# Optimization experiments

Hardware: AMD Instinct MI355X
Metric: run time of the kernel (lower is better)

## Reference

```python
import jax, jax.numpy as jnp
import numpy as np

B, S, DIM = 2, 2048, 2048
H, QLR, KVLR = 16, 1536, 512
D_NOPE, D_ROPE, D_QK, D_V = 128, 64, 192, 128
EPS = 1e-6


def rms_norm(x, w, eps=EPS):
    return x * jax.lax.rsqrt(jnp.mean(jnp.square(x), axis=-1, keepdims=True) + eps) * w


def rope(x, theta):
    # x: [b, s, n, d], theta: [s, d//2] rotation angles
    xr = x.reshape(*x.shape[:-1], -1, 2)
    x0, x1 = xr[..., 0], xr[..., 1]
    cos = jnp.cos(theta)[None, :, None, :]
    sin = jnp.sin(theta)[None, :, None, :]
    out = jnp.stack([x0 * cos - x1 * sin, x0 * sin + x1 * cos], axis=-1)
    return out.reshape(x.shape).astype(x.dtype)


def setup_inputs() -> dict:
    key = jax.random.key(0)
    ks = jax.random.split(key, 6)
    x = jax.random.normal(ks[0], (B, S, DIM), jnp.float32)
    # standard RoPE angles theta[s, i] = s / 10000^(2i/d_rope)
    pos = jnp.arange(S, dtype=jnp.float32)
    inv = 1.0 / (10000.0 ** (jnp.arange(0, D_ROPE, 2, dtype=jnp.float32) / D_ROPE))
    freqs = pos[:, None] * inv[None, :]  # [S, D_ROPE//2]
    sc = lambda k, shp: jax.random.normal(k, shp, jnp.float32) * (1.0 / np.sqrt(shp[0]))
    return {
        'x': x,
        'freqs': freqs,
        'start_pos': 0,
        'wq_a': sc(ks[1], (DIM, QLR)),
        'q_norm_w': jnp.ones((QLR,), jnp.float32),
        'wq_b': sc(ks[2], (QLR, H * D_QK)),
        'wkv_a': sc(ks[3], (DIM, KVLR + D_ROPE)),
        'kv_norm_w': jnp.ones((KVLR,), jnp.float32),
        'wkv_b': sc(ks[4], (KVLR, H * (D_NOPE + D_V))),
        'wo': sc(ks[5], (H * D_V, DIM)),
    }


def reference(x, freqs, start_pos, wq_a, q_norm_w, wq_b, wkv_a, kv_norm_w, wkv_b, wo):
    bsz, seqlen, _ = x.shape
    scale = D_QK ** -0.5
    # low-rank Q: down-proj -> RMSNorm -> up-proj
    q = rms_norm(x @ wq_a, q_norm_w) @ wq_b
    q = q.reshape(bsz, seqlen, H, D_QK)
    q_nope, q_pe = q[..., :D_NOPE], q[..., D_NOPE:]
    q_pe = rope(q_pe, freqs)
    # low-rank KV: joint down-proj, split latent / rope part
    kv = x @ wkv_a
    c_kv, k_pe = kv[..., :KVLR], kv[..., KVLR:]
    k_pe = rope(k_pe[:, :, None, :], freqs)[:, :, 0, :]  # [b, t, r]
    # weight absorption: fold wkv_b's k_nope block into q
    wkv_b_mat = wkv_b.T.reshape(H, D_NOPE + D_V, KVLR)  # [h, d_nope+d_v, c]
    q_abs = jnp.einsum('bshd,hdc->bshc', q_nope, wkv_b_mat[:, :D_NOPE])
    kv_cache = rms_norm(c_kv, kv_norm_w)  # [b, t, c] compressed KV cache
    scores = (jnp.einsum('bshc,btc->bsht', q_abs, kv_cache)
              + jnp.einsum('bshr,btr->bsht', q_pe, k_pe)) * scale
    causal = jnp.tril(jnp.ones((seqlen, seqlen), bool))  # prefill, start_pos=0
    scores = jnp.where(causal[None, :, None, :], scores, -1e9)
    attn = jax.nn.softmax(scores.astype(jnp.float32), axis=-1).astype(x.dtype)
    # attend in latent space, then up-project with the v block of wkv_b
    o = jnp.einsum('bsht,btc->bshc', attn, kv_cache)
    o = jnp.einsum('bshc,hdc->bshd', o, wkv_b_mat[:, D_NOPE:])
    return o.reshape(bsz, seqlen, H * D_V) @ wo
```

## Files before the change

kernel.cpp:

```cpp
#include <hip/hip_runtime.h>

typedef __bf16 bf16x8 __attribute__((ext_vector_type(8)));
typedef float floatx4 __attribute__((ext_vector_type(4)));

#define MFMA(a, b, c) __builtin_amdgcn_mfma_f32_16x16x32_bf16((a), (b), (c), 0, 0, 0)

__device__ __forceinline__ float bf2f(ushort u) {
    union { unsigned int i; float f; } v; v.i = ((unsigned int)u) << 16; return v.f;
}
__device__ __forceinline__ ushort f2bf(float f) {
    union { float f; unsigned int i; } v; v.f = f;
    unsigned int r = v.i + 0x7fffu + ((v.i >> 16) & 1u);
    return (ushort)(r >> 16);
}
__device__ __forceinline__ ushort f2bf_n(float f) {
    union { __bf16 b; ushort u; } v; v.b = (__bf16)f; return v.u;
}
__device__ __forceinline__ bf16x8 ldb8(const ushort* p) { return *(const bf16x8*)p; }

__global__ __launch_bounds__(256) void transpose_f32_bf16(
    const float* __restrict__ in, ushort* __restrict__ out, int R, int C) {
    __shared__ ushort tile[32][33];
    const int c0 = blockIdx.x * 32, r0 = blockIdx.y * 32;
    const int tx = threadIdx.x, ty = threadIdx.y;
    #pragma unroll
    for (int i = 0; i < 32; i += 8) {
        int r = r0 + ty + i, c = c0 + tx;
        if (r < R && c < C) tile[ty + i][tx] = f2bf(in[(long)r * C + c]);
    }
    __syncthreads();
    #pragma unroll
    for (int i = 0; i < 32; i += 8) {
        int r = c0 + ty + i, c = r0 + tx;
        if (r < C && c < R) out[(long)r * R + c] = tile[tx][ty + i];
    }
}

__global__ __launch_bounds__(256) void cvt_f32_bf16(
    const float* __restrict__ in, ushort* __restrict__ out, long n) {
    const long i = ((long)blockIdx.x * 256 + threadIdx.x) * 4;
    if (i >= n) return;
    float4 v = *(const float4*)(in + i);
    ushort4 o;
    o.x = f2bf(v.x); o.y = f2bf(v.y); o.z = f2bf(v.z); o.w = f2bf(v.w);
    *(ushort4*)(out + i) = o;
}

__global__ __launch_bounds__(256) void trigtab(
    const float* __restrict__ freqs, float2* __restrict__ trig) {
    const int idx = blockIdx.x * 256 + threadIdx.x;
    float th = freqs[idx];
    trig[idx] = make_float2(cosf(th), sinf(th));
}

__global__ __launch_bounds__(256, 3) void gemm_bt128(
    const ushort* __restrict__ A, const ushort* __restrict__ Bt,
    void* __restrict__ C, int K, int lda, int ldb, int ldc,
    long aZ, long bZ, long cZ, int c_f32) {
    __shared__ __align__(16) ushort As[128 * 64];
    __shared__ __align__(16) ushort Bs[128 * 64];
    const int z = blockIdx.z;
    const ushort* Ab = A + (long)z * aZ;
    const ushort* Bb = Bt + (long)z * bZ;
    const long m0 = (long)blockIdx.y * 128;
    const long n0 = (long)blockIdx.x * 128;
    const int tid = threadIdx.x;
    const int lane = tid & 63, w = tid >> 6;
    const int wm = (w >> 1) * 64, wn = (w & 1) * 64;
    const int lrow = lane & 15, quad = lane >> 4;

    floatx4 acc[4][4] = {};

    for (int k0 = 0; k0 < K; k0 += 64) {
        __syncthreads();
        #pragma unroll
        for (int t = 0; t < 4; ++t) {
            const int c = t * 256 + tid;
            const int r = c >> 3, kc = (c & 7) * 8;
            __builtin_amdgcn_global_load_lds(
                (const __attribute__((address_space(1))) unsigned int*)(Ab + (m0 + r) * lda + k0 + kc),
                (__attribute__((address_space(3))) unsigned int*)(As + (long)c * 8), 16, 0, 0);
            __builtin_amdgcn_global_load_lds(
                (const __attribute__((address_space(1))) unsigned int*)(Bb + (n0 + r) * ldb + k0 + kc),
                (__attribute__((address_space(3))) unsigned int*)(Bs + (long)c * 8), 16, 0, 0);
        }
        __syncthreads();
        #pragma unroll
        for (int kk = 0; kk < 64; kk += 32) {
            bf16x8 af[4], bv[4];
            #pragma unroll
            for (int i = 0; i < 4; ++i) {
                af[i] = ldb8(&As[(wm + i * 16 + lrow) * 64 + kk + quad * 8]);
                bv[i] = ldb8(&Bs[(wn + i * 16 + lrow) * 64 + kk + quad * 8]);
            }
            #pragma unroll
            for (int i = 0; i < 4; ++i)
                #pragma unroll
                for (int j = 0; j < 4; ++j)
                    acc[i][j] = MFMA(af[i], bv[j], acc[i][j]);
        }
    }
    if (c_f32) {
        float* Cb = (float*)C + (long)z * cZ;
        #pragma unroll
        for (int mt = 0; mt < 4; ++mt)
            #pragma unroll
            for (int nt = 0; nt < 4; ++nt)
                #pragma unroll
                for (int r = 0; r < 4; ++r)
                    Cb[(m0 + wm + mt * 16 + quad * 4 + r) * ldc + n0 + wn + nt * 16 + lrow] = acc[mt][nt][r];
    } else {
        ushort* Cb = (ushort*)C + (long)z * cZ;
        #pragma unroll
        for (int mt = 0; mt < 4; ++mt)
            #pragma unroll
            for (int nt = 0; nt < 4; ++nt)
                #pragma unroll
                for (int r = 0; r < 4; ++r)
                    Cb[(m0 + wm + mt * 16 + quad * 4 + r) * ldc + n0 + wn + nt * 16 + lrow] = f2bf(acc[mt][nt][r]);
    }
}

__global__ __launch_bounds__(256) void rms1536(
    ushort* qk, const float* __restrict__ w) {
    const int row = blockIdx.x, t = threadIdx.x;
    const int lane = t & 63, wv = t >> 6;
    ushort* ip = qk + (long)row * 2176;
    float v[6]; float ss = 0.f;
    #pragma unroll
    for (int i = 0; i < 6; ++i) { v[i] = bf2f(ip[i * 256 + t]); ss += v[i] * v[i]; }
    #pragma unroll
    for (int off = 32; off > 0; off >>= 1) ss += __shfl_xor(ss, off);
    __shared__ float red[4];
    if (lane == 0) red[wv] = ss;
    __syncthreads();
    const float tot = red[0] + red[1] + red[2] + red[3];
    const float sc = rsqrtf(tot * (1.f / 1536.f) + 1e-6f);
    #pragma unroll
    for (int i = 0; i < 6; ++i) ip[i * 256 + t] = f2bf(v[i] * sc * w[i * 256 + t]);
}

__global__ __launch_bounds__(256) void qrope(
    const ushort* __restrict__ q, const float2* __restrict__ trig,
    ushort* __restrict__ qpe) {
    const int tok = blockIdx.x;
    const int s = tok & 2047;
    const int t = threadIdx.x;
    #pragma unroll
    for (int p = 0; p < 2; ++p) {
        const int idx = p * 256 + t;
        const int h = idx >> 5, i = idx & 31;
        const long base = (long)tok * 3072 + h * 192 + 128 + 2 * i;
        float x0 = bf2f(q[base]), x1 = bf2f(q[base + 1]);
        float2 cs = trig[s * 32 + i];
        const long ob = (long)tok * 1024 + h * 64 + 2 * i;
        qpe[ob]     = f2bf(x0 * cs.x - x1 * cs.y);
        qpe[ob + 1] = f2bf(x0 * cs.y + x1 * cs.x);
    }
}

__global__ __launch_bounds__(256) void kvprep(
    const ushort* __restrict__ qk, const float* __restrict__ w,
    const float2* __restrict__ trig, ushort* __restrict__ kvc,
    ushort* __restrict__ kpe) {
    const int tok = blockIdx.x;
    const int s = tok & 2047;
    const int t = threadIdx.x;
    const int lane = t & 63, wv = t >> 6;
    const ushort* in2 = qk + (long)tok * 2176 + 1536;
    const float v0 = bf2f(in2[t]);
    const float v1 = bf2f(in2[256 + t]);
    float ss = v0 * v0 + v1 * v1;
    #pragma unroll
    for (int off = 32; off > 0; off >>= 1) ss += __shfl_xor(ss, off);
    __shared__ float red[4];
    if (lane == 0) red[wv] = ss;
    __syncthreads();
    const float tot = red[0] + red[1] + red[2] + red[3];
    const float sc = rsqrtf(tot * (1.f / 512.f) + 1e-6f);
    kvc[(long)tok * 512 + t] = f2bf(v0 * sc * w[t]);
    kvc[(long)tok * 512 + 256 + t] = f2bf(v1 * sc * w[256 + t]);
    if (t < 32) {
        float x0 = bf2f(in2[512 + 2 * t]);
        float x1 = bf2f(in2[512 + 2 * t + 1]);
        float2 cs = trig[s * 32 + t];
        kpe[(long)tok * 64 + 2 * t]     = f2bf(x0 * cs.x - x1 * cs.y);
        kpe[(long)tok * 64 + 2 * t + 1] = f2bf(x0 * cs.y + x1 * cs.x);
    }
}

__global__ __launch_bounds__(256, 2) void mha_attn(
    const ushort* __restrict__ q,
    const ushort* __restrict__ qpe,
    const ushort* __restrict__ kn,
    const ushort* __restrict__ kpe,
    const ushort* __restrict__ vT,
    ushort* __restrict__ o2) {
    __shared__ __align__(16) ushort Ks[128][200];
    __shared__ __align__(16) ushort P[64][136];
    const int fid = blockIdx.x + (blockIdx.y << 4) + (blockIdx.z << 8);
    const int xcd = fid & 7, j = fid >> 3;
    const int g = xcd * 4 + (j >> 4);
    const int qx = j & 15, h = g & 15, b = g >> 4;
    const int tid = threadIdx.x, lane = tid & 63, w = tid >> 6;
    const int lrow = lane & 15, quad = lane >> 4;
    const long bb = (long)b * 2048;
    const float scale = 0.07216878364870323f * 1.4426950408889634f;
    const int rn = tid >> 4, cn = (tid & 15) * 8;
    const int rr = tid >> 3, cr = (tid & 7) * 8;

    for (int half = 0; half < 2; ++half) {
        const int qt = half ? (31 - qx) : qx;
        const int qrow = qt * 64;
        const long tokb = bb + qrow;

        bf16x8 qa[6];
        {
            const ushort* qp_ = q + (tokb + w * 16 + lrow) * 3072 + h * 192 + quad * 8;
            #pragma unroll
            for (int ks = 0; ks < 4; ++ks) qa[ks] = ldb8(qp_ + ks * 32);
            const ushort* qq = qpe + (tokb + w * 16 + lrow) * 1024 + h * 64 + quad * 8;
            qa[4] = ldb8(qq); qa[5] = ldb8(qq + 32);
        }

        floatx4 oacc[4][2] = {};
        float m_i[4], l_i[4];
        #pragma unroll
        for (int r = 0; r < 4; ++r) { m_i[r] = -1e30f; l_i[r] = 0.f; }

        const int niter = qt / 2 + 1;
        for (int t = 0; t < niter; ++t) {
            const int kv0 = t * 128;
            {
                const ushort* src = kn + (bb + kv0 + rn) * 2048 + h * 128 + cn;
                #pragma unroll
                for (int j2 = 0; j2 < 8; ++j2) {
                    uint4 v = *(const uint4*)(src + (long)j2 * 16 * 2048);
                    *(uint4*)&Ks[j2 * 16 + rn][cn] = v;
                }
                const ushort* srp = kpe + (bb + kv0 + rr) * 64 + cr;
                #pragma unroll
                for (int j2 = 0; j2 < 4; ++j2) {
                    uint4 v = *(const uint4*)(srp + (long)j2 * 32 * 64);
                    *(uint4*)&Ks[j2 * 32 + rr][128 + cr] = v;
                }
            }
            __syncthreads();

            floatx4 sacc[8] = {};
            __builtin_amdgcn_s_setprio(1);
            #pragma unroll
            for (int f = 0; f < 8; ++f)
                #pragma unroll
                for (int ks = 0; ks < 6; ++ks)
                    sacc[f] = MFMA(qa[ks], ldb8(&Ks[f * 16 + lrow][ks * 32 + quad * 8]), sacc[f]);
            __builtin_amdgcn_s_setprio(0);

            bf16x8 vf[2][4];
            {
                const ushort* vb = vT + ((long)(b * 16 + h)) * 262144 + (long)(w * 32 + lrow) * 2048 + kv0 + quad * 8;
                #pragma unroll
                for (int nf = 0; nf < 2; ++nf)
                    #pragma unroll
                    for (int kk = 0; kk < 4; ++kk)
                        vf[nf][kk] = ldb8(vb + (long)nf * 16 * 2048 + kk * 32);
            }

            const bool diag = (t == niter - 1);
            #pragma unroll
            for (int r = 0; r < 4; ++r) {
                const int rloc = w * 16 + quad * 4 + r;
                const int row_s = qrow + rloc;
                float pv[8];
                float smax = -1e30f;
                #pragma unroll
                for (int f = 0; f < 8; ++f) {
                    pv[f] = sacc[f][r] * scale;
                    if (diag) { if (kv0 + f * 16 + lrow > row_s) pv[f] = -1e30f; }
                    smax = fmaxf(smax, pv[f]);
                }
                #pragma unroll
                for (int off = 1; off < 16; off <<= 1)
                    smax = fmaxf(smax, __shfl_xor(smax, off));
                const float mnew = fmaxf(m_i[r], smax);
                const float alpha = __builtin_amdgcn_exp2f(m_i[r] - mnew);
                float ps = 0.f;
                #pragma unroll
                for (int f = 0; f < 8; ++f) {
                    float p = __builtin_amdgcn_exp2f(pv[f] - mnew);
                    P[rloc][f * 16 + lrow] = f2bf_n(p);
                    ps += p;
                }
                #pragma unroll
                for (int off = 1; off < 16; off <<= 1)
                    ps += __shfl_xor(ps, off);
                l_i[r] = l_i[r] * alpha + ps;
                m_i[r] = mnew;
                if (lrow == 0) *(float*)&P[rloc][128] = alpha;
            }
            __syncthreads();

            __builtin_amdgcn_s_setprio(1);
            #pragma unroll
            for (int mf = 0; mf < 4; ++mf) {
                float al[4];
                #pragma unroll
                for (int r = 0; r < 4; ++r) al[r] = *(const float*)&P[mf * 16 + quad * 4 + r][128];
                const int need = (al[0] != 1.f) | (al[1] != 1.f) | (al[2] != 1.f) | (al[3] != 1.f);
                if (__any(need)) {
                    #pragma unroll
                    for (int nf = 0; nf < 2; ++nf)
                        #pragma unroll
                        for (int r = 0; r < 4; ++r) oacc[mf][nf][r] *= al[r];
                }
                #pragma unroll
                for (int kk = 0; kk < 4; ++kk) {
                    bf16x8 pf = ldb8(&P[mf * 16 + lrow][kk * 32 + quad * 8]);
                    oacc[mf][0] = MFMA(pf, vf[0][kk], oacc[mf][0]);
                    oacc[mf][1] = MFMA(pf, vf[1][kk], oacc[mf][1]);
                }
            }
            __builtin_amdgcn_s_setprio(0);
        }

        #pragma unroll
        for (int r = 0; r < 4; ++r)
            if (lrow == 0) *(float*)&P[w * 16 + quad * 4 + r][132] = l_i[r];
        __syncthreads();
        #pragma unroll
        for (int mf = 0; mf < 4; ++mf) {
            float li[4];
            #pragma unroll
            for (int r = 0; r < 4; ++r) li[r] = *(const float*)&P[mf * 16 + quad * 4 + r][132];
            #pragma unroll
            for (int nf = 0; nf < 2; ++nf)
                #pragma unroll
                for (int r = 0; r < 4; ++r) {
                    long tok = tokb + mf * 16 + quad * 4 + r;
                    o2[tok * 2048 + h * 128 + w * 32 + nf * 16 + lrow] = f2bf_n(oacc[mf][nf][r] / li[r]);
                }
        }
        __syncthreads();
    }
}

extern "C" void kernel_launch(void* const* d_in, const int* in_sizes, int n_in,
                              void* d_out, int out_size, void* d_ws, size_t ws_size,
                              hipStream_t stream) {
    const float* x      = (const float*)d_in[0];
    const float* freqs  = (const float*)d_in[1];
    const float* wq_a   = (const float*)d_in[3];
    const float* qnw    = (const float*)d_in[4];
    const float* wq_b   = (const float*)d_in[5];
    const float* wkv_a  = (const float*)d_in[6];
    const float* kvnw   = (const float*)d_in[7];
    const float* wkv_b  = (const float*)d_in[8];
    const float* wo     = (const float*)d_in[9];
    float* out = (float*)d_out;
    (void)ws_size; (void)in_sizes; (void)n_in; (void)out_size;

    char* ws = (char*)d_ws;
    ushort* qk_comb = (ushort*)(ws + 0);
    ushort* o2      = (ushort*)(ws + 0);
    ushort* xb      = (ushort*)(ws + 17825792);
    ushort* knope   = (ushort*)(ws + 17825792);
    ushort* q       = (ushort*)(ws + 34603008);
    ushort* qpe     = (ushort*)(ws + 59768832);
    ushort* kvc     = (ushort*)(ws + 68157440);
    ushort* kpe     = (ushort*)(ws + 72351744);
    ushort* vT      = (ushort*)(ws + 72876032);
    ushort* wcombT  = (ushort*)(ws + 89653248);
    ushort* wq_bT   = (ushort*)(ws + 98566144);
    ushort* wkv_bT  = (ushort*)(ws + 108003328);
    ushort* woT     = (ushort*)(ws + 112197632);
    float2* trig    = (float2*)(ws + 120586240);

    dim3 tb(32, 8);
    trigtab<<<256, 256, 0, stream>>>(freqs, trig);
    transpose_f32_bf16<<<dim3(48, 64), tb, 0, stream>>>(wq_a, wcombT, 2048, 1536);
    transpose_f32_bf16<<<dim3(18, 64), tb, 0, stream>>>(wkv_a, wcombT + 1536L * 2048, 2048, 576);
    transpose_f32_bf16<<<dim3(96, 48), tb, 0, stream>>>(wq_b, wq_bT, 1536, 3072);
    transpose_f32_bf16<<<dim3(128, 16), tb, 0, stream>>>(wkv_b, wkv_bT, 512, 4096);
    transpose_f32_bf16<<<dim3(64, 64), tb, 0, stream>>>(wo, woT, 2048, 2048);
    cvt_f32_bf16<<<8192, 256, 0, stream>>>(x, xb, 8388608L);

    gemm_bt128<<<dim3(17, 32, 1), 256, 0, stream>>>(xb, wcombT, qk_comb, 2048, 2048, 2048, 2176, 0, 0, 0, 0);
    rms1536<<<4096, 256, 0, stream>>>(qk_comb, qnw);
    gemm_bt128<<<dim3(24, 32, 1), 256, 0, stream>>>(qk_comb, wq_bT, q, 1536, 2176, 1536, 3072, 0, 0, 0, 0);
    qrope<<<4096, 256, 0, stream>>>(q, trig, qpe);
    kvprep<<<4096, 256, 0, stream>>>(qk_comb, kvnw, trig, kvc, kpe);

    gemm_bt128<<<dim3(1, 32, 16), 256, 0, stream>>>(kvc, wkv_bT, knope,
        512, 512, 512, 2048, 0, 131072, 128, 0);
    gemm_bt128<<<dim3(16, 1, 16), 256, 0, stream>>>(wkv_bT + 65536, kvc, vT,
        512, 512, 512, 2048, 131072, 0, 262144, 0);
    gemm_bt128<<<dim3(16, 1, 16), 256, 0, stream>>>(wkv_bT + 65536, kvc + 1048576, vT + 4194304,
        512, 512, 512, 2048, 131072, 0, 262144, 0);

    mha_attn<<<dim3(16, 16, 2), 256, 0, stream>>>(q, qpe, knope, kpe, vT, o2);

    gemm_bt128<<<dim3(16, 32, 1), 256, 0, stream>>>(o2, woT, out, 2048, 2048, 2048, 2048, 0, 0, 0, 1);
}
```

Measured before the change: 479.3 us.

## Merge per-batch V up-projection GEMMs and add lazy softmax max rescaling

Replaces the two per-batch V-projection GEMM launches with one dedicated gemm_vt kernel that covers both batches through blockIdx.z, loading tiles into LDS with global_load_lds and allowing three blocks per CU. In the attention kernel, the running max is only updated when the new tile max exceeds the old one by a threshold, so exp2 arguments stay bounded and alpha is usually exactly one. The aim is to save one launch plus tail effects and to cut rescaling work in the softmax loop. The lazy max lets unnormalized probabilities grow up to 2^11.5 before the final division, which relies on fp32 and bf16 P having enough headroom.

Measured after the change: 471.6 us. About the same (-1.6%).

```diff
diff --git a/kernel.cpp b/kernel.cpp
--- a/kernel.cpp
+++ b/kernel.cpp
@@ -119,6 +119,61 @@
                 for (int r = 0; r < 4; ++r)
                     Cb[(m0 + wm + mt * 16 + quad * 4 + r) * ldc + n0 + wn + nt * 16 + lrow] = f2bf(acc[mt][nt][r]);
     }
+}
+
+__global__ __launch_bounds__(256, 3) void gemm_vt(
+    const ushort* __restrict__ Wb, const ushort* __restrict__ kvc,
+    ushort* __restrict__ vT) {
+    __shared__ __align__(16) ushort As[128 * 64];
+    __shared__ __align__(16) ushort Bs[128 * 64];
+    const int z = blockIdx.z, b = z >> 4, h = z & 15;
+    const ushort* Ab = Wb + (long)h * 131072;
+    const ushort* Bb = kvc + (long)b * 1048576;
+    ushort* Cb = vT + (long)b * 4194304 + (long)h * 262144;
+    const long n0 = (long)blockIdx.x * 128;
+    const int tid = threadIdx.x;
+    const int lane = tid & 63, w = tid >> 6;
+    const int wm = (w >> 1) * 64, wn = (w & 1) * 64;
+    const int lrow = lane & 15, quad = lane >> 4;
+
+    floatx4 acc[4][4] = {};
+
+    for (int k0 = 0; k0 < 512; k0 += 64) {
+        __syncthreads();
+        #pragma unroll
+        for (int t = 0; t < 4; ++t) {
+            const int c = t * 256 + tid;
+            const int r = c >> 3, kc = (c & 7) * 8;
+            __builtin_amdgcn_global_load_lds(
+                (const __attribute__((address_space(1))) unsigned int*)(Ab + (long)r * 512 + k0 + kc),
+                (__attribute__((address_space(3))) unsigned int*)(As + (long)c * 8), 16, 0, 0);
+            __builtin_amdgcn_global_load_lds(
+                (const __attribute__((address_space(1))) unsigned int*)(Bb + (n0 + r) * 512 + k0 + kc),
+                (__attribute__((address_space(3))) unsigned int*)(Bs + (long)c * 8), 16, 0, 0);
+        }
+        __syncthreads();
+        #pragma unroll
+        for (int kk = 0; kk < 64; kk += 32) {
+            bf16x8 af[4], bv[4];
+            #pragma unroll
+            for (int i = 0; i < 4; ++i) {
+                af[i] = ldb8(&As[(wm + i * 16 + lrow) * 64 + kk + quad * 8]);
+                bv[i] = ldb8(&Bs[(wn + i * 16 + lrow) * 64 + kk + quad * 8]);
+            }
+            #pragma unroll
+            for (int i = 0; i < 4; ++i)
+                #pragma unroll
+                for (int j = 0; j < 4; ++j)
+                    acc[i][j] = MFMA(af[i], bv[j], acc[i][j]);
+        }
+    }
+    #pragma unroll
+    for (int mt = 0; mt < 4; ++mt)
+        #pragma unroll
+        for (int nt = 0; nt < 4; ++nt)
+            #pragma unroll
+            for (int r = 0; r < 4; ++r)
+                Cb[(long)(wm + mt * 16 + quad * 4 + r) * 2048 + n0 + wn + nt * 16 + lrow] = f2bf(acc[mt][nt][r]);
 }
 
 __global__ __launch_bounds__(256) void rms1536(
@@ -206,6 +261,7 @@
     const int lrow = lane & 15, quad = lane >> 4;
     const long bb = (long)b * 2048;
     const float scale = 0.07216878364870323f * 1.4426950408889634f;
+    const float THR = 11.5417f;
     const int rn = tid >> 4, cn = (tid & 15) * 8;
     const int rr = tid >> 3, cr = (tid & 7) * 8;
 
@@ -282,7 +338,7 @@
                 #pragma unroll
                 for (int off = 1; off < 16; off <<= 1)
                     smax = fmaxf(smax, __shfl_xor(smax, off));
-                const float mnew = fmaxf(m_i[r], smax);
+                const float mnew = (smax > m_i[r] + THR) ? smax : m_i[r];
                 const float alpha = __builtin_amdgcn_exp2f(m_i[r] - mnew);
                 float ps = 0.f;
                 #pragma unroll
@@ -392,10 +448,7 @@
 
     gemm_bt128<<<dim3(1, 32, 16), 256, 0, stream>>>(kvc, wkv_bT, knope,
         512, 512, 512, 2048, 0, 131072, 128, 0);
-    gemm_bt128<<<dim3(16, 1, 16), 256, 0, stream>>>(wkv_bT + 65536, kvc, vT,
-        512, 512, 512, 2048, 131072, 0, 262144, 0);
-    gemm_bt128<<<dim3(16, 1, 16), 256, 0, stream>>>(wkv_bT + 65536, kvc + 1048576, vT + 4194304,
-        512, 512, 512, 2048, 131072, 0, 262144, 0);
+    gemm_vt<<<dim3(16, 1, 32), 256, 0, stream>>>(wkv_bT + 65536, kvc, vT);
 
     mha_attn<<<dim3(16, 16, 2), 256, 0, stream>>>(q, qpe, knope, kpe, vT, o2);
 
```
